# Performance work log

Hardware: AMD Instinct MI355X
Metric: run time of the kernel (lower is better)

The kernel has to match this reference:

```python
import jax, jax.numpy as jnp
import numpy as np

N, E, G = 100000, 1600000, 16
GW = 128
EPS = 1e-5        # BatchNorm eps
MIN_SCORE = 0.1   # TopK min_score
TOL = 1e-7        # PyG topk tolerance
NEG = -1e9


def _seg_sum(v, idx, n):
    return jax.ops.segment_sum(v, idx, num_segments=n)


def _seg_max(v, idx, n):
    return jax.ops.segment_max(v, idx, num_segments=n)


def setup_inputs():
    ks = jax.random.split(jax.random.key(0), 32)
    inp = {}
    inp['x'] = jax.random.normal(ks[0], (N, 2), jnp.float32)
    inp['edge_index'] = jax.random.randint(ks[1], (2, E), 0, N, jnp.int32)
    inp['batch_index'] = jnp.sort(jax.random.randint(ks[2], (N,), 0, G, jnp.int32))
    inp['gcn_w'] = jax.random.normal(ks[3], (2, 1), jnp.float32) / np.sqrt(2.0)
    inp['gcn_b'] = jax.random.normal(ks[4], (1,), jnp.float32) * 0.1
    inp['topk_w'] = jax.random.normal(ks[5], (1,), jnp.float32)
    dims = [(2, GW), (GW, GW), (GW, GW)]
    j = 6
    for i, (din, dout) in enumerate(dims):
        s = 1.0 / np.sqrt(din)
        inp[f'cheb{i}_w0'] = jax.random.normal(ks[j], (din, dout), jnp.float32) * s; j += 1
        inp[f'cheb{i}_w1'] = jax.random.normal(ks[j], (din, dout), jnp.float32) * s; j += 1
        inp[f'cheb{i}_b'] = jax.random.normal(ks[j], (dout,), jnp.float32) * 0.1; j += 1
    inp['bn_gamma'] = jax.random.uniform(ks[j], (3, GW), jnp.float32) + 0.5; j += 1
    inp['bn_beta'] = jax.random.normal(ks[j], (3, GW), jnp.float32) * 0.1; j += 1
    inp['bn_mean'] = jax.random.normal(ks[j], (3, GW), jnp.float32) * 0.1; j += 1
    inp['bn_var'] = jax.random.uniform(ks[j], (3, GW), jnp.float32) + 0.5; j += 1
    for name, (din, dout) in [('lin0', (3 * GW, 32)), ('lin1', (32, 8)), ('linf', (8, 3))]:
        s = 1.0 / np.sqrt(din)
        inp[f'{name}_w'] = jax.random.normal(ks[j], (din, dout), jnp.float32) * s; j += 1
        inp[f'{name}_b'] = jax.random.normal(ks[j], (dout,), jnp.float32) * s; j += 1
    return inp


def reference(x, edge_index, batch_index, gcn_w, gcn_b, topk_w,
              cheb0_w0, cheb0_w1, cheb0_b, cheb1_w0, cheb1_w1, cheb1_b,
              cheb2_w0, cheb2_w1, cheb2_b, bn_gamma, bn_beta, bn_mean, bn_var,
              lin0_w, lin0_b, lin1_w, lin1_b, linf_w, linf_b):
    src, dst = edge_index[0], edge_index[1]

    # --- CustomGCN(2,1): sym-normalized A+I (frozen weights), out [N,1] ---
    xw = x @ gcn_w                                  # [N,1]
    deg = _seg_sum(jnp.ones(E, x.dtype), dst, N) + 1.0   # +1 self loop
    dinv = jax.lax.rsqrt(deg)
    agg = _seg_sum(xw[src] * (dinv[src] * dinv[dst])[:, None], dst, N)
    attn = agg + xw * (dinv * dinv)[:, None] + gcn_b

    # --- CustomTopK(1, min_score=0.1): per-graph softmax, keep > min(max-tol, 0.1) ---
    s_raw = (attn * topk_w).sum(-1)                 # [N]
    smax = _seg_max(s_raw, batch_index, G)
    ex = jnp.exp(s_raw - smax[batch_index])
    score = ex / _seg_sum(ex, batch_index, G)[batch_index]
    thr = jnp.minimum(_seg_max(score, batch_index, G) - TOL, MIN_SCORE)[batch_index]
    mask = score > thr                              # [N] kept nodes
    fm = mask.astype(x.dtype)
    h = x * score[:, None] * fm[:, None]            # x[perm] * score[perm], masked form

    # edges surviving the pooling (both endpoints kept)
    em = fm[src] * fm[dst]                          # [E]
    degf = _seg_sum(em, dst, N)
    dinvf = jnp.where(degf > 0, jax.lax.rsqrt(jnp.maximum(degf, 1.0)), 0.0)
    normf = dinvf[src] * dinvf[dst] * em            # [E] sym-norm on filtered graph

    def cheb(h, w0, w1, b):
        # K=2, lambda_max=2: Tx1 = (L_hat) h = -D^-1/2 A D^-1/2 h
        tx1 = -_seg_sum(h[src] * normf[:, None], dst, N)
        return h @ w0 + tx1 @ w1 + b

    def bn(h, i):
        return (h - bn_mean[i]) * (bn_gamma[i] * jax.lax.rsqrt(bn_var[i] + EPS)) + bn_beta[i]

    mneg = jnp.where(mask[:, None], 0.0, NEG)       # mask dropped nodes out of gmp
    xs = []
    for i, (w0, w1, b) in enumerate([(cheb0_w0, cheb0_w1, cheb0_b),
                                     (cheb1_w0, cheb1_w1, cheb1_b),
                                     (cheb2_w0, cheb2_w1, cheb2_b)]):
        h = jax.nn.elu(cheb(h, w0, w1, b))
        h = bn(h, i)
        xs.append(jnp.maximum(_seg_max(h + mneg, batch_index, G), NEG))
    g = jnp.concatenate(xs, axis=1)                 # [G, 3*GW]

    g = jax.nn.elu(g @ lin0_w + lin0_b)
    g = jax.nn.elu(g @ lin1_w + lin1_b)
    # dropout is identity in eval mode
    g = g @ linf_w + linf_b
    return jax.nn.log_softmax(g, axis=1)
```

## Files before the change

kernel.cpp:

```cpp
#include <hip/hip_runtime.h>
#include <math.h>

#define NG 16
#define GW 128
#define NEGV -1.0e9f
#define EPSBN 1e-5f
#define MIN_SCORE 0.1f
#define TOLK 1e-7f
#define NBIN 1024
#define NPBMAX 256
#define EPT 16
#define KCAP 256
#define ECAP 2048
#define ROWCAP 16
#define LECAP 256

__device__ __forceinline__ unsigned encf(float f) {
  unsigned u = __float_as_uint(f);
  return (u & 0x80000000u) ? ~u : (u | 0x80000000u);
}
__device__ __forceinline__ float decf(unsigned u) {
  unsigned b = (u & 0x80000000u) ? (u & 0x7fffffffu) : ~u;
  return __uint_as_float(b);
}
__device__ __forceinline__ float eluf(float v) { return v > 0.0f ? v : expm1f(v); }

__global__ void k_zero(int* __restrict__ bincnt, int* __restrict__ counters,
                       unsigned* __restrict__ smax_e, float* __restrict__ sumex) {
  int t = threadIdx.x;
  for (int i = t; i < NBIN; i += blockDim.x) bincnt[i] = 0;
  if (t < NG) { smax_e[t] = encf(-INFINITY); sumex[t] = 0.0f; }
  if (t == 0) { counters[0] = 0; counters[1] = 0; }
}

__global__ __launch_bounds__(1024) void k_scatter(
    const int* __restrict__ src, const int* __restrict__ dst, int ne, int shift,
    int cap, int* __restrict__ bincnt, unsigned* __restrict__ sorted,
    const float* __restrict__ x, const float* __restrict__ gcn_w,
    float* __restrict__ xw, int n) {
  __shared__ int lh[NBIN];
  __shared__ int gb[NBIN];
  int t = threadIdx.x;
  long gid = (long)blockIdx.x * 1024 + t;
  long gs = (long)gridDim.x * 1024;
  float w0 = gcn_w[0], w1 = gcn_w[1];
  for (long i = gid; i < n; i += gs) xw[i] = x[2 * i] * w0 + x[2 * i + 1] * w1;
  for (int b = t; b < NBIN; b += 1024) lh[b] = 0;
  __syncthreads();
  long ebase = (long)blockIdx.x * (1024 * EPT);
  int rank[EPT], dv[EPT];
  #pragma unroll
  for (int k = 0; k < EPT; ++k) {
    long e = ebase + (long)k * 1024 + t;
    rank[k] = 0; dv[k] = 0;
    if (e < ne) { dv[k] = dst[e]; rank[k] = atomicAdd(&lh[dv[k] >> shift], 1); }
  }
  __syncthreads();
  for (int b = t; b < NBIN; b += 1024)
    gb[b] = lh[b] ? atomicAdd(&bincnt[b], lh[b]) : 0;
  __syncthreads();
  #pragma unroll
  for (int k = 0; k < EPT; ++k) {
    long e = ebase + (long)k * 1024 + t;
    if (e < ne) {
      int d = dv[k], bin = d >> shift;
      int pos = gb[bin] + rank[k];
      if (pos < cap)
        sorted[(size_t)bin * cap + pos] =
            ((unsigned)(d & ((1 << shift) - 1)) << 24) | (unsigned)src[e];
    }
  }
}

__global__ void k_c1(const unsigned* __restrict__ sorted, const int* __restrict__ bincnt,
                     int cap, const float* __restrict__ xw, float* __restrict__ dinv,
                     float* __restrict__ y, int n, int shift) {
  __shared__ int ldeg[NPBMAX];
  int b = blockIdx.x;
  int off = b << shift;
  if (off >= n) return;
  int npb = 1 << shift;
  int t = threadIdx.x;
  for (int j = t; j < npb; j += blockDim.x) ldeg[j] = 0;
  __syncthreads();
  size_t s0 = (size_t)b * cap;
  int cnt = bincnt[b]; if (cnt > cap) cnt = cap;
  for (int i = t; i < cnt; i += blockDim.x)
    atomicAdd(&ldeg[sorted[s0 + i] >> 24], 1);
  __syncthreads();
  for (int j = t; j < npb; j += blockDim.x) {
    int g = off + j;
    if (g < n) {
      float dv = rsqrtf((float)(ldeg[j] + 1));
      dinv[g] = dv;
      y[g] = xw[g] * dv;
    }
  }
}

__global__ void k_c2(const unsigned* __restrict__ sorted, const int* __restrict__ bincnt,
                     int cap, const float* __restrict__ y, const float* __restrict__ xw,
                     const float* __restrict__ dinv, const int* __restrict__ batch,
                     const float* __restrict__ gcn_b, const float* __restrict__ topk_w,
                     float* __restrict__ s_raw, unsigned* __restrict__ smax_e,
                     float* __restrict__ sumex, int n, int shift) {
  __shared__ float lt[NPBMAX];
  __shared__ unsigned ls[NG];
  __shared__ float lsum[NG];
  int b = blockIdx.x;
  int off = b << shift;
  if (off >= n) return;
  int npb = 1 << shift;
  int t = threadIdx.x;
  for (int j = t; j < npb; j += blockDim.x) lt[j] = 0.0f;
  if (t < NG) { ls[t] = encf(-INFINITY); lsum[t] = 0.0f; }
  __syncthreads();
  size_t s0 = (size_t)b * cap;
  int cnt = bincnt[b]; if (cnt > cap) cnt = cap;
  for (int i = t; i < cnt; i += blockDim.x) {
    unsigned p = sorted[s0 + i];
    atomicAdd(&lt[p >> 24], y[p & 0xFFFFFFu]);
  }
  __syncthreads();
  float gb_ = gcn_b[0], tw = topk_w[0];
  for (int j = t; j < npb; j += blockDim.x) {
    int g = off + j;
    if (g < n) {
      float dv = dinv[g];
      float attn = dv * lt[j] + xw[g] * dv * dv + gb_;
      float s = attn * tw;
      s_raw[g] = s;
      int bb = batch[g];
      atomicMax(&ls[bb], encf(s));
      atomicAdd(&lsum[bb], expf(s));
    }
  }
  __syncthreads();
  if (t < NG) {
    if (ls[t] != encf(-INFINITY)) atomicMax(&smax_e[t], ls[t]);
    if (lsum[t] != 0.0f) atomicAdd(&sumex[t], lsum[t]);
  }
}

__global__ void k_compact_n(const float* __restrict__ s_raw, const float* __restrict__ sumex,
                            const unsigned* __restrict__ smax_e,
                            const int* __restrict__ batch, const float* __restrict__ x,
                            int* __restrict__ kmap, int* __restrict__ kbatch,
                            float* __restrict__ hk, float* __restrict__ degfc,
                            int* __restrict__ counters, int n) {
  int i = blockIdx.x * blockDim.x + threadIdx.x;
  if (i >= n) return;
  if (i < KCAP) degfc[i] = 0.0f;
  int b = batch[i];
  float se = sumex[b];
  float score = expf(s_raw[i]) / se;
  float ms = expf(decf(smax_e[b])) / se;
  float thr = fminf(ms - TOLK, MIN_SCORE);
  int m = -1;
  if (score > thr) {
    int idx = atomicAdd(&counters[0], 1);
    if (idx < KCAP) {
      m = idx;
      kbatch[idx] = b;
      hk[2 * idx]     = x[2 * i] * score;
      hk[2 * idx + 1] = x[2 * i + 1] * score;
    }
  }
  kmap[i] = m;
}

__global__ void k_compact_e(const unsigned* __restrict__ sorted, const int* __restrict__ bincnt,
                            int cap, const int* __restrict__ kmap,
                            int* __restrict__ eks, int* __restrict__ ekd,
                            float* __restrict__ degfc, int* __restrict__ counters,
                            int n, int shift) {
  int b = blockIdx.x;
  int off = b << shift;
  if (off >= n) return;
  size_t s0 = (size_t)b * cap;
  int cnt = bincnt[b]; if (cnt > cap) cnt = cap;
  for (int i = threadIdx.x; i < cnt; i += blockDim.x) {
    unsigned p = sorted[s0 + i];
    int ks = kmap[p & 0xFFFFFFu];
    if (ks < 0) continue;
    int kd = kmap[off + (int)(p >> 24)];
    if (kd < 0) continue;
    int j = atomicAdd(&counters[1], 1);
    if (j < ECAP) {
      eks[j] = ks;
      ekd[j] = kd;
      atomicAdd(&degfc[kd], 1.0f);
    }
  }
}

__device__ void tail_layer(const float* hin, float* tx, float* hout,
                           const float* __restrict__ w0, const float* __restrict__ w1,
                           const float* __restrict__ cb,
                           const float* __restrict__ bng, const float* __restrict__ bnb,
                           const float* __restrict__ bnm, const float* __restrict__ bnv,
                           int L, int R, int LE, int S, bool fast,
                           const int* les, const int* led, const float* lenf,
                           const int* kl, const int* rows_g,
                           const int* __restrict__ kbatch,
                           const int* __restrict__ eks, const int* __restrict__ ekd,
                           const float* __restrict__ degfc,
                           unsigned* lgm, int g, int t) {
  for (int i = t; i < R * GW; i += 256) tx[i] = 0.0f;
  __syncthreads();
  if (fast) {
    for (int idx = t; idx < LE * GW; idx += 256) {
      int e = idx >> 7, c = idx & 127;
      int sr = kl[les[e]];
      if (sr >= 0) atomicAdd(&tx[led[e] * GW + c], -hin[sr * GW + c] * lenf[e]);
    }
  } else {
    for (int e = t; e < S; e += 256) {
      int kd = ekd[e];
      int dr = kl[kd];
      if (dr < 0) continue;
      int sr = kl[eks[e]];
      if (sr < 0) continue;
      float dfs = degfc[eks[e]], dfd = degfc[kd];
      float nf = (dfs > 0.f ? rsqrtf(dfs) : 0.f) * (dfd > 0.f ? rsqrtf(dfd) : 0.f);
      for (int c = 0; c < GW; ++c)
        atomicAdd(&tx[dr * GW + c], -hin[sr * GW + c] * nf);
    }
  }
  __syncthreads();
  int j = t & 127, ih = t >> 7;
  float sc = bng[L * GW + j] * rsqrtf(bnv[L * GW + j] + EPSBN);
  float mn = bnm[L * GW + j], bt = bnb[L * GW + j], bj = cb[j];
  for (int i = ih; i < R; i += 2) {
    float acc = bj;
    for (int k = 0; k < GW; ++k)
      acc += hin[i * GW + k] * w0[k * GW + j] + tx[i * GW + k] * w1[k * GW + j];
    float v = eluf(acc);
    v = (v - mn) * sc + bt;
    if (hout) hout[i * GW + j] = v;
    if (kbatch[rows_g[i]] == g) atomicMax(&lgm[L * GW + j], encf(v));
  }
  __syncthreads();
}

__global__ __launch_bounds__(256) void k_tail(
    const float* __restrict__ hk, const int* __restrict__ kbatch,
    const int* __restrict__ counters,
    const int* __restrict__ eks, const int* __restrict__ ekd,
    const float* __restrict__ degfc,
    const float* __restrict__ c0w0, const float* __restrict__ c0w1, const float* __restrict__ c0b,
    const float* __restrict__ c1w0, const float* __restrict__ c1w1, const float* __restrict__ c1b,
    const float* __restrict__ c2w0, const float* __restrict__ c2w1, const float* __restrict__ c2b,
    const float* __restrict__ bng, const float* __restrict__ bnb,
    const float* __restrict__ bnm, const float* __restrict__ bnv,
    const float* __restrict__ l0w, const float* __restrict__ l0b,
    const float* __restrict__ l1w, const float* __restrict__ l1b,
    const float* __restrict__ lfw, const float* __restrict__ lfb,
    float* __restrict__ g_hA, float* __restrict__ g_hB, float* __restrict__ g_tx,
    float* __restrict__ g_t0, float* __restrict__ out) {
  __shared__ float sA[ROWCAP * GW], sB[ROWCAP * GW], sT[ROWCAP * GW];
  __shared__ float t0v[ROWCAP * 2];
  __shared__ int kl[KCAP];
  __shared__ int rows_g[KCAP];
  __shared__ int les[LECAP], led[LECAP];
  __shared__ float lenf[LECAP];
  __shared__ unsigned lgm[3 * GW];
  __shared__ int cnts[2];
  __shared__ float mlp0[32], mlp1[8], lg3[3];

  int g = blockIdx.x, t = threadIdx.x;
  int K = counters[0]; if (K > KCAP) K = KCAP;
  int S = counters[1]; if (S > ECAP) S = ECAP;
  if (t == 0) { cnts[0] = 0; cnts[1] = 0; }
  for (int i = t; i < KCAP; i += 256) kl[i] = -1;
  for (int i = t; i < 3 * GW; i += 256) lgm[i] = encf(NEGV);
  __syncthreads();
  for (int i = t; i < K; i += 256)
    if (kbatch[i] == g) { int r = atomicAdd(&cnts[0], 1); rows_g[r] = i; }
  __syncthreads();
  int R0 = cnts[0];
  for (int r = t; r < R0; r += 256) kl[rows_g[r]] = r;
  __syncthreads();
  if (t == 0) {
    for (int pass = 0; pass < 2; ++pass) {
      int Rcur = cnts[0];
      for (int e = 0; e < S; ++e) {
        int kd = ekd[e];
        if (kl[kd] >= 0 && kl[kd] < Rcur) {
          int ks = eks[e];
          if (kl[ks] < 0) { int r = cnts[0]++; rows_g[r] = ks; kl[ks] = r; }
        }
      }
    }
  }
  __syncthreads();
  int R = cnts[0];
  for (int e = t; e < S; e += 256) {
    int kd = ekd[e];
    if (kl[kd] >= 0) {
      int j = atomicAdd(&cnts[1], 1);
      if (j < LECAP) {
        les[j] = eks[e];
        led[j] = kl[kd];
        float dfs = degfc[eks[e]], dfd = degfc[kd];
        lenf[j] = (dfs > 0.f ? rsqrtf(dfs) : 0.f) * (dfd > 0.f ? rsqrtf(dfd) : 0.f);
      }
    }
  }
  __syncthreads();
  int LE = cnts[1]; if (LE > LECAP) LE = LECAP;
  bool fast = (R <= ROWCAP) && (cnts[1] <= LECAP);
  float* hA  = fast ? sA  : g_hA + (size_t)g * KCAP * GW;
  float* hB  = fast ? sB  : g_hB + (size_t)g * KCAP * GW;
  float* tx  = fast ? sT  : g_tx + (size_t)g * KCAP * GW;
  float* t0p = fast ? t0v : g_t0 + (size_t)g * KCAP * 2;

  for (int i = t; i < R * 2; i += 256) t0p[i] = 0.0f;
  __syncthreads();
  if (fast) {
    for (int idx = t; idx < LE * 2; idx += 256) {
      int e = idx >> 1, c = idx & 1;
      atomicAdd(&t0p[led[e] * 2 + c], -hk[les[e] * 2 + c] * lenf[e]);
    }
  } else {
    for (int e = t; e < S; e += 256) {
      int kd = ekd[e];
      int dr = kl[kd];
      if (dr < 0) continue;
      int ks = eks[e];
      float dfs = degfc[ks], dfd = degfc[kd];
      float nf = (dfs > 0.f ? rsqrtf(dfs) : 0.f) * (dfd > 0.f ? rsqrtf(dfd) : 0.f);
      atomicAdd(&t0p[dr * 2],     -hk[ks * 2] * nf);
      atomicAdd(&t0p[dr * 2 + 1], -hk[ks * 2 + 1] * nf);
    }
  }
  __syncthreads();
  {
    int j = t & 127, ih = t >> 7;
    float sc = bng[j] * rsqrtf(bnv[j] + EPSBN);
    float mn = bnm[j], bt = bnb[j];
    for (int i = ih; i < R; i += 2) {
      int gi = rows_g[i];
      float acc = c0b[j] + hk[gi * 2] * c0w0[j] + hk[gi * 2 + 1] * c0w0[GW + j]
                + t0p[i * 2] * c0w1[j] + t0p[i * 2 + 1] * c0w1[GW + j];
      float v = eluf(acc);
      v = (v - mn) * sc + bt;
      hA[i * GW + j] = v;
      if (kbatch[gi] == g) atomicMax(&lgm[j], encf(v));
    }
  }
  __syncthreads();
  tail_layer(hA, tx, hB, c1w0, c1w1, c1b, bng, bnb, bnm, bnv, 1, R, LE, S, fast,
             les, led, lenf, kl, rows_g, kbatch, eks, ekd, degfc, lgm, g, t);
  tail_layer(hB, tx, nullptr, c2w0, c2w1, c2b, bng, bnb, bnm, bnv, 2, R, LE, S, fast,
             les, led, lenf, kl, rows_g, kbatch, eks, ekd, degfc, lgm, g, t);
  if (t < 32) {
    float acc = l0b[t];
    for (int k = 0; k < 3 * GW; ++k) acc += decf(lgm[k]) * l0w[k * 32 + t];
    mlp0[t] = eluf(acc);
  }
  __syncthreads();
  if (t < 8) {
    float acc = l1b[t];
    for (int k = 0; k < 32; ++k) acc += mlp0[k] * l1w[k * 8 + t];
    mlp1[t] = eluf(acc);
  }
  __syncthreads();
  if (t < 3) {
    float acc = lfb[t];
    for (int k = 0; k < 8; ++k) acc += mlp1[k] * lfw[k * 3 + t];
    lg3[t] = acc;
  }
  __syncthreads();
  if (t == 0) {
    float a = lg3[0], b = lg3[1], c = lg3[2];
    float m = fmaxf(a, fmaxf(b, c));
    float ls = m + logf(expf(a - m) + expf(b - m) + expf(c - m));
    out[g * 3 + 0] = a - ls;
    out[g * 3 + 1] = b - ls;
    out[g * 3 + 2] = c - ls;
  }
}

extern "C" void kernel_launch(void* const* d_in, const int* in_sizes, int n_in,
                              void* d_out, int out_size, void* d_ws, size_t ws_size,
                              hipStream_t stream) {
  const float* x      = (const float*)d_in[0];
  const int*   ei     = (const int*)d_in[1];
  const int*   batch  = (const int*)d_in[2];
  const float* gcn_w  = (const float*)d_in[3];
  const float* gcn_b  = (const float*)d_in[4];
  const float* topk_w = (const float*)d_in[5];
  const float* c0w0 = (const float*)d_in[6],  *c0w1 = (const float*)d_in[7],  *c0b = (const float*)d_in[8];
  const float* c1w0 = (const float*)d_in[9],  *c1w1 = (const float*)d_in[10], *c1b = (const float*)d_in[11];
  const float* c2w0 = (const float*)d_in[12], *c2w1 = (const float*)d_in[13], *c2b = (const float*)d_in[14];
  const float* bng = (const float*)d_in[15], *bnb = (const float*)d_in[16];
  const float* bnm = (const float*)d_in[17], *bnv = (const float*)d_in[18];
  const float* l0w = (const float*)d_in[19], *l0b = (const float*)d_in[20];
  const float* l1w = (const float*)d_in[21], *l1b = (const float*)d_in[22];
  const float* lfw = (const float*)d_in[23], *lfb = (const float*)d_in[24];
  float* out = (float*)d_out;

  const int n  = in_sizes[2];
  const int ne = in_sizes[1] / 2;
  const int* src = ei;
  const int* dst = ei + ne;

  int shift = 0;
  while (((n - 1) >> shift) >= NBIN) shift++;
  if (shift > 8) shift = 8;
  const int nbins = ((n - 1) >> shift) + 1;
  int avg = (ne + nbins - 1) / nbins;
  int cap = avg + (int)(8.0 * sqrt((double)avg)) + 64;
  cap = (cap + 15) & ~15;

  char* bp = (char*)d_ws;
  size_t off = 0;
  auto A = [&](size_t bytes) -> void* {
    void* r = (void*)(bp + off);
    off += (bytes + 255) & ~(size_t)255;
    return r;
  };
  float*    xw     = (float*)A((size_t)n * 4);
  float*    dinv   = (float*)A((size_t)n * 4);
  float*    y      = (float*)A((size_t)n * 4);
  float*    s_raw  = (float*)A((size_t)n * 4);
  int*      kmap   = (int*)A((size_t)n * 4);
  unsigned* sorted = (unsigned*)A((size_t)NBIN * cap * 4);
  int*      bincnt = (int*)A(NBIN * 4);
  unsigned* smax_e = (unsigned*)A(NG * 4);
  float*    sumex  = (float*)A(NG * 4);
  int*      counters = (int*)A(8);
  int*      kbatch = (int*)A((size_t)KCAP * 4);
  float*    degfc  = (float*)A((size_t)KCAP * 4);
  float*    hk     = (float*)A((size_t)KCAP * 8);
  int*      eks    = (int*)A((size_t)ECAP * 4);
  int*      ekd    = (int*)A((size_t)ECAP * 4);
  float*    g_hA   = (float*)A((size_t)NG * KCAP * GW * 4);
  float*    g_hB   = (float*)A((size_t)NG * KCAP * GW * 4);
  float*    g_tx   = (float*)A((size_t)NG * KCAP * GW * 4);
  float*    g_t0   = (float*)A((size_t)NG * KCAP * 8);

  const int nbN = (n + 255) / 256;
  const int nbS = (ne + 1024 * EPT - 1) / (1024 * EPT);

  k_zero<<<1, 1024, 0, stream>>>(bincnt, counters, smax_e, sumex);
  k_scatter<<<nbS, 1024, 0, stream>>>(src, dst, ne, shift, cap, bincnt, sorted,
                                      x, gcn_w, xw, n);
  k_c1<<<NBIN, 256, 0, stream>>>(sorted, bincnt, cap, xw, dinv, y, n, shift);
  k_c2<<<NBIN, 256, 0, stream>>>(sorted, bincnt, cap, y, xw, dinv, batch, gcn_b,
                                 topk_w, s_raw, smax_e, sumex, n, shift);
  k_compact_n<<<nbN, 256, 0, stream>>>(s_raw, sumex, smax_e, batch, x, kmap,
                                       kbatch, hk, degfc, counters, n);
  k_compact_e<<<NBIN, 256, 0, stream>>>(sorted, bincnt, cap, kmap, eks, ekd,
                                        degfc, counters, n, shift);
  k_tail<<<NG, 256, 0, stream>>>(hk, kbatch, counters, eks, ekd, degfc,
                                 c0w0, c0w1, c0b, c1w0, c1w1, c1b, c2w0, c2w1, c2b,
                                 bng, bnb, bnm, bnv, l0w, l0b, l1w, l1b, lfw, lfb,
                                 g_hA, g_hB, g_tx, g_t0, out);
}
```

Measured before the change: 102.1 us.

## Stage Chebyshev and MLP weights in LDS with register-blocked rows in tail kernel

Splits the tail's fast path into a templated layer routine. It stages each 128x128 weight matrix into shared memory and accumulates up to 8 rows per thread in registers, so each weight element is read once per layer rather than once per row from global memory. The final MLP also stages lin0/lin1/linf weights in shared memory and splits the 384-long lin0 dot product across all 256 threads with a shared reduction. This adds 64KB of shared memory, which may limit occupancy, but k_tail runs only 16 blocks.

```diff
diff --git a/kernel.cpp b/kernel.cpp
--- a/kernel.cpp
+++ b/kernel.cpp
@@ -24,6 +24,13 @@
   return __uint_as_float(b);
 }
 __device__ __forceinline__ float eluf(float v) { return v > 0.0f ? v : expm1f(v); }
+
+__device__ __forceinline__ void stage_w(const float* __restrict__ w, float* wbuf, int t) {
+  const float4* w4 = (const float4*)w;
+  float4* b4 = (float4*)wbuf;
+  #pragma unroll
+  for (int i = 0; i < 16; ++i) b4[t + 256 * i] = w4[t + 256 * i];
+}
 
 __global__ void k_zero(int* __restrict__ bincnt, int* __restrict__ counters,
                        unsigned* __restrict__ smax_e, float* __restrict__ sumex) {
@@ -194,38 +201,29 @@
   }
 }
 
-__device__ void tail_layer(const float* hin, float* tx, float* hout,
-                           const float* __restrict__ w0, const float* __restrict__ w1,
-                           const float* __restrict__ cb,
-                           const float* __restrict__ bng, const float* __restrict__ bnb,
-                           const float* __restrict__ bnm, const float* __restrict__ bnv,
-                           int L, int R, int LE, int S, bool fast,
-                           const int* les, const int* led, const float* lenf,
-                           const int* kl, const int* rows_g,
-                           const int* __restrict__ kbatch,
-                           const int* __restrict__ eks, const int* __restrict__ ekd,
-                           const float* __restrict__ degfc,
-                           unsigned* lgm, int g, int t) {
+__device__ void tail_layer_slow(const float* hin, float* tx, float* hout,
+                                const float* __restrict__ w0, const float* __restrict__ w1,
+                                const float* __restrict__ cb,
+                                const float* __restrict__ bng, const float* __restrict__ bnb,
+                                const float* __restrict__ bnm, const float* __restrict__ bnv,
+                                int L, int R, int S,
+                                const int* kl, const int* rows_g,
+                                const int* __restrict__ kbatch,
+                                const int* __restrict__ eks, const int* __restrict__ ekd,
+                                const float* __restrict__ degfc,
+                                unsigned* lgm, int g, int t) {
   for (int i = t; i < R * GW; i += 256) tx[i] = 0.0f;
   __syncthreads();
-  if (fast) {
-    for (int idx = t; idx < LE * GW; idx += 256) {
-      int e = idx >> 7, c = idx & 127;
-      int sr = kl[les[e]];
-      if (sr >= 0) atomicAdd(&tx[led[e] * GW + c], -hin[sr * GW + c] * lenf[e]);
-    }
-  } else {
-    for (int e = t; e < S; e += 256) {
-      int kd = ekd[e];
-      int dr = kl[kd];
-      if (dr < 0) continue;
-      int sr = kl[eks[e]];
-      if (sr < 0) continue;
-      float dfs = degfc[eks[e]], dfd = degfc[kd];
-      float nf = (dfs > 0.f ? rsqrtf(dfs) : 0.f) * (dfd > 0.f ? rsqrtf(dfd) : 0.f);
-      for (int c = 0; c < GW; ++c)
-        atomicAdd(&tx[dr * GW + c], -hin[sr * GW + c] * nf);
-    }
+  for (int e = t; e < S; e += 256) {
+    int kd = ekd[e];
+    int dr = kl[kd];
+    if (dr < 0) continue;
+    int sr = kl[eks[e]];
+    if (sr < 0) continue;
+    float dfs = degfc[eks[e]], dfd = degfc[kd];
+    float nf = (dfs > 0.f ? rsqrtf(dfs) : 0.f) * (dfd > 0.f ? rsqrtf(dfd) : 0.f);
+    for (int c = 0; c < GW; ++c)
+      atomicAdd(&tx[dr * GW + c], -hin[sr * GW + c] * nf);
   }
   __syncthreads();
   int j = t & 127, ih = t >> 7;
@@ -239,6 +237,56 @@
     v = (v - mn) * sc + bt;
     if (hout) hout[i * GW + j] = v;
     if (kbatch[rows_g[i]] == g) atomicMax(&lgm[L * GW + j], encf(v));
+  }
+  __syncthreads();
+}
+
+template <int MR>
+__device__ void layer_fast(const float* hin, const float* txl, float* hout,
+                           const float* __restrict__ w0g, const float* __restrict__ w1g,
+                           const float* __restrict__ cb,
+                           const float* __restrict__ bng, const float* __restrict__ bnb,
+                           const float* __restrict__ bnm, const float* __restrict__ bnv,
+                           int L, int R, const int* rows_g,
+                           const int* __restrict__ kbatch,
+                           unsigned* lgm, float* wbuf, int g, int t) {
+  int j = t & 127, ih = t >> 7;
+  float bj = cb[j];
+  float acc[MR];
+  #pragma unroll
+  for (int r = 0; r < MR; ++r) acc[r] = bj;
+  stage_w(w0g, wbuf, t);
+  __syncthreads();
+  for (int k = 0; k < GW; ++k) {
+    float wv = wbuf[k * GW + j];
+    #pragma unroll
+    for (int r = 0; r < MR; ++r) {
+      int row = ih + 2 * r;
+      if (row < R) acc[r] += hin[row * GW + k] * wv;
+    }
+  }
+  __syncthreads();
+  stage_w(w1g, wbuf, t);
+  __syncthreads();
+  for (int k = 0; k < GW; ++k) {
+    float wv = wbuf[k * GW + j];
+    #pragma unroll
+    for (int r = 0; r < MR; ++r) {
+      int row = ih + 2 * r;
+      if (row < R) acc[r] += txl[row * GW + k] * wv;
+    }
+  }
+  float sc = bng[L * GW + j] * rsqrtf(bnv[L * GW + j] + EPSBN);
+  float mn = bnm[L * GW + j], bt = bnb[L * GW + j];
+  #pragma unroll
+  for (int r = 0; r < MR; ++r) {
+    int row = ih + 2 * r;
+    if (row < R) {
+      float v = eluf(acc[r]);
+      v = (v - mn) * sc + bt;
+      if (hout) hout[row * GW + j] = v;
+      if (kbatch[rows_g[row]] == g) atomicMax(&lgm[L * GW + j], encf(v));
+    }
   }
   __syncthreads();
 }
@@ -258,6 +306,7 @@
     const float* __restrict__ lfw, const float* __restrict__ lfb,
     float* __restrict__ g_hA, float* __restrict__ g_hB, float* __restrict__ g_tx,
     float* __restrict__ g_t0, float* __restrict__ out) {
+  __shared__ float wbuf[GW * GW];
   __shared__ float sA[ROWCAP * GW], sB[ROWCAP * GW], sT[ROWCAP * GW];
   __shared__ float t0v[ROWCAP * 2];
   __shared__ int kl[KCAP];
@@ -266,6 +315,7 @@
   __shared__ float lenf[LECAP];
   __shared__ unsigned lgm[3 * GW];
   __shared__ int cnts[2];
+  __shared__ float red[256];
   __shared__ float mlp0[32], mlp1[8], lg3[3];
 
   int g = blockIdx.x, t = threadIdx.x;
@@ -310,19 +360,65 @@
   __syncthreads();
   int LE = cnts[1]; if (LE > LECAP) LE = LECAP;
   bool fast = (R <= ROWCAP) && (cnts[1] <= LECAP);
-  float* hA  = fast ? sA  : g_hA + (size_t)g * KCAP * GW;
-  float* hB  = fast ? sB  : g_hB + (size_t)g * KCAP * GW;
-  float* tx  = fast ? sT  : g_tx + (size_t)g * KCAP * GW;
-  float* t0p = fast ? t0v : g_t0 + (size_t)g * KCAP * 2;
-
-  for (int i = t; i < R * 2; i += 256) t0p[i] = 0.0f;
-  __syncthreads();
+
   if (fast) {
+    for (int i = t; i < R * 2; i += 256) t0v[i] = 0.0f;
+    __syncthreads();
     for (int idx = t; idx < LE * 2; idx += 256) {
       int e = idx >> 1, c = idx & 1;
-      atomicAdd(&t0p[led[e] * 2 + c], -hk[les[e] * 2 + c] * lenf[e]);
-    }
+      atomicAdd(&t0v[led[e] * 2 + c], -hk[les[e] * 2 + c] * lenf[e]);
+    }
+    __syncthreads();
+    {
+      int j = t & 127, ih = t >> 7;
+      float sc = bng[j] * rsqrtf(bnv[j] + EPSBN);
+      float mn = bnm[j], bt = bnb[j];
+      for (int i = ih; i < R; i += 2) {
+        int gi = rows_g[i];
+        float acc = c0b[j] + hk[gi * 2] * c0w0[j] + hk[gi * 2 + 1] * c0w0[GW + j]
+                  + t0v[i * 2] * c0w1[j] + t0v[i * 2 + 1] * c0w1[GW + j];
+        float v = eluf(acc);
+        v = (v - mn) * sc + bt;
+        sA[i * GW + j] = v;
+        if (kbatch[gi] == g) atomicMax(&lgm[j], encf(v));
+      }
+    }
+    __syncthreads();
+    for (int i = t; i < R * GW; i += 256) sT[i] = 0.0f;
+    __syncthreads();
+    for (int idx = t; idx < LE * GW; idx += 256) {
+      int e = idx >> 7, c = idx & 127;
+      int sr = kl[les[e]];
+      if (sr >= 0) atomicAdd(&sT[led[e] * GW + c], -sA[sr * GW + c] * lenf[e]);
+    }
+    __syncthreads();
+    if (R <= 2)
+      layer_fast<1>(sA, sT, sB, c1w0, c1w1, c1b, bng, bnb, bnm, bnv, 1, R,
+                    rows_g, kbatch, lgm, wbuf, g, t);
+    else
+      layer_fast<8>(sA, sT, sB, c1w0, c1w1, c1b, bng, bnb, bnm, bnv, 1, R,
+                    rows_g, kbatch, lgm, wbuf, g, t);
+    for (int i = t; i < R * GW; i += 256) sT[i] = 0.0f;
+    __syncthreads();
+    for (int idx = t; idx < LE * GW; idx += 256) {
+      int e = idx >> 7, c = idx & 127;
+      int sr = kl[les[e]];
+      if (sr >= 0) atomicAdd(&sT[led[e] * GW + c], -sB[sr * GW + c] * lenf[e]);
+    }
+    __syncthreads();
+    if (R <= 2)
+      layer_fast<1>(sB, sT, nullptr, c2w0, c2w1, c2b, bng, bnb, bnm, bnv, 2, R,
+                    rows_g, kbatch, lgm, wbuf, g, t);
+    else
+      layer_fast<8>(sB, sT, nullptr, c2w0, c2w1, c2b, bng, bnb, bnm, bnv, 2, R,
+                    rows_g, kbatch, lgm, wbuf, g, t);
   } else {
+    float* hA  = g_hA + (size_t)g * KCAP * GW;
+    float* hB  = g_hB + (size_t)g * KCAP * GW;
+    float* tx  = g_tx + (size_t)g * KCAP * GW;
+    float* t0p = g_t0 + (size_t)g * KCAP * 2;
+    for (int i = t; i < R * 2; i += 256) t0p[i] = 0.0f;
+    __syncthreads();
     for (int e = t; e < S; e += 256) {
       int kd = ekd[e];
       int dr = kl[kd];
@@ -333,42 +429,62 @@
       atomicAdd(&t0p[dr * 2],     -hk[ks * 2] * nf);
       atomicAdd(&t0p[dr * 2 + 1], -hk[ks * 2 + 1] * nf);
     }
-  }
-  __syncthreads();
+    __syncthreads();
+    {
+      int j = t & 127, ih = t >> 7;
+      float sc = bng[j] * rsqrtf(bnv[j] + EPSBN);
+      float mn = bnm[j], bt = bnb[j];
+      for (int i = ih; i < R; i += 2) {
+        int gi = rows_g[i];
+        float acc = c0b[j] + hk[gi * 2] * c0w0[j] + hk[gi * 2 + 1] * c0w0[GW + j]
+                  + t0p[i * 2] * c0w1[j] + t0p[i * 2 + 1] * c0w1[GW + j];
+        float v = eluf(acc);
+        v = (v - mn) * sc + bt;
+        hA[i * GW + j] = v;
+        if (kbatch[gi] == g) atomicMax(&lgm[j], encf(v));
+      }
+    }
+    __syncthreads();
+    tail_layer_slow(hA, tx, hB, c1w0, c1w1, c1b, bng, bnb, bnm, bnv, 1, R, S,
+                    kl, rows_g, kbatch, eks, ekd, degfc, lgm, g, t);
+    tail_layer_slow(hB, tx, nullptr, c2w0, c2w1, c2b, bng, bnb, bnm, bnv, 2, R, S,
+                    kl, rows_g, kbatch, eks, ekd, degfc, lgm, g, t);
+  }
+
   {
-    int j = t & 127, ih = t >> 7;
-    float sc = bng[j] * rsqrtf(bnv[j] + EPSBN);
-    float mn = bnm[j], bt = bnb[j];
-    for (int i = ih; i < R; i += 2) {
-      int gi = rows_g[i];
-      float acc = c0b[j] + hk[gi * 2] * c0w0[j] + hk[gi * 2 + 1] * c0w0[GW + j]
-                + t0p[i * 2] * c0w1[j] + t0p[i * 2 + 1] * c0w1[GW + j];
-      float v = eluf(acc);
-      v = (v - mn) * sc + bt;
-      hA[i * GW + j] = v;
-      if (kbatch[gi] == g) atomicMax(&lgm[j], encf(v));
-    }
-  }
-  __syncthreads();
-  tail_layer(hA, tx, hB, c1w0, c1w1, c1b, bng, bnb, bnm, bnv, 1, R, LE, S, fast,
-             les, led, lenf, kl, rows_g, kbatch, eks, ekd, degfc, lgm, g, t);
-  tail_layer(hB, tx, nullptr, c2w0, c2w1, c2b, bng, bnb, bnm, bnv, 2, R, LE, S, fast,
-             les, led, lenf, kl, rows_g, kbatch, eks, ekd, degfc, lgm, g, t);
+    const float4* a4 = (const float4*)l0w;
+    float4* b4 = (float4*)wbuf;
+    #pragma unroll
+    for (int i = 0; i < 12; ++i) b4[t + 256 * i] = a4[t + 256 * i];
+    wbuf[12288 + t] = l1w[t & 255];
+    if (t < 24) wbuf[12544 + t] = lfw[t];
+  }
+  __syncthreads();
+  {
+    int jo = t & 31, kb = t >> 5;
+    float a = 0.f;
+    for (int kk = 0; kk < 48; ++kk) {
+      int k = kb * 48 + kk;
+      a += decf(lgm[k]) * wbuf[k * 32 + jo];
+    }
+    red[t] = a;
+  }
+  __syncthreads();
   if (t < 32) {
     float acc = l0b[t];
-    for (int k = 0; k < 3 * GW; ++k) acc += decf(lgm[k]) * l0w[k * 32 + t];
+    for (int b2 = 0; b2 < 8; ++b2) acc += red[b2 * 32 + t];
     mlp0[t] = eluf(acc);
   }
   __syncthreads();
   if (t < 8) {
     float acc = l1b[t];
-    for (int k = 0; k < 32; ++k) acc += mlp0[k] * l1w[k * 8 + t];
+    for (int k = 0; k < 32; ++k) acc += mlp0[k] * wbuf[12288 + k * 8 + t];
     mlp1[t] = eluf(acc);
   }
   __syncthreads();
   if (t < 3) {
     float acc = lfb[t];
-    for (int k = 0; k < 8; ++k) acc += mlp1[k] * lfw[k * 3 + t];
+    for (int k = 0; k < 8; ++k) acc += mlp1[k] * wbuf[12544 + k * 3 + t];
     lg3[t] = acc;
   }
   __syncthreads();
```

New measurement: 103.3 us. About the same (+1.2%).
